# Kernel tuning notes

Measured on AMD Instinct MI355X. Metric: run time of the kernel, lower is better.

## Reference

```python
import jax, jax.numpy as jnp
import numpy as np

MARGIN = 0.2
NEG_INF = -1e9  # safe stand-in for -inf when masking the max


def setup_inputs() -> dict:
    key = jax.random.key(0)
    k1, k2, k3 = jax.random.split(key, 3)
    B, D = 8192, 256
    p = jax.random.normal(k1, (B, D), dtype=jnp.float32)
    # module docstring says projections are normalized
    projections = p / jnp.linalg.norm(p, axis=1, keepdims=True)
    affordance_ids = jax.random.randint(k2, (B,), 0, 36, dtype=jnp.int64)
    instance_ids = jax.random.randint(k3, (B,), 0, 2048, dtype=jnp.int64)
    return {
        "projections": projections,
        "affordance_ids": affordance_ids,
        "instance_ids": instance_ids,
    }


def reference(projections, affordance_ids, instance_ids):
    # (B, B) cosine similarities
    sim = jnp.matmul(projections, projections.T)

    aff_eq = affordance_ids[:, None] == affordance_ids[None, :]
    inst_eq = instance_ids[:, None] == instance_ids[None, :]
    pos_mask = aff_eq & ~inst_eq          # same affordance, different instance
    neg_mask = ~aff_eq                    # different affordance

    # per-row hard negative: max similarity over negatives
    hard_neg = jnp.max(jnp.where(neg_mask, sim, NEG_INF), axis=1)  # (B,)

    # rows contribute only if they have >=1 positive AND >=1 negative
    valid_row = pos_mask.any(axis=1) & neg_mask.any(axis=1)        # (B,)
    pair_mask = pos_mask & valid_row[:, None]                      # (B, B)

    # margin loss for every (anchor i, positive j) pair
    losses = jnp.maximum(hard_neg[:, None] - sim + MARGIN, 0.0)

    total = jnp.sum(jnp.where(pair_mask, losses, 0.0))
    num_pairs = jnp.sum(pair_mask)
    return jnp.where(num_pairs > 0, total / num_pairs, 0.0)
```

## Files before the change

### kernel.cpp

```cpp
#include <hip/hip_runtime.h>

#define NB 8192
#define ND 256
#define NCLS 64
#define LOSS_MARGIN 0.2f
#define NEG_INF_F (-1e9f)
#define LMAXT 3
#define NBLK_LOSS (NCLS * LMAXT * LMAXT)
#define NTILE_T 2080

typedef __attribute__((ext_vector_type(8))) __bf16 bf16x8;
typedef __attribute__((ext_vector_type(4))) float f32x4;

__device__ __forceinline__ unsigned short f2bf(float f) {
  unsigned u = __float_as_uint(f);
  unsigned r = (u + 0x7fffu + ((u >> 16) & 1u)) >> 16;
  return (unsigned short)r;
}

__device__ __forceinline__ void gl_lds16(const void* gsrc, void* ldst) {
  __builtin_amdgcn_global_load_lds(
      (const __attribute__((address_space(1))) void*)gsrc,
      (__attribute__((address_space(3))) void*)ldst, 16, 0, 0);
}

__global__ __launch_bounds__(1024) void build_idx_fused(const int* __restrict__ aff,
                                                        int* __restrict__ class_start,
                                                        int* __restrict__ class_idx) {
  const int c = blockIdx.x;
  const int t = threadIdx.x;
  const int lane = t & 63, wave = t >> 6;
  __shared__ int wtot[16];
  __shared__ int s_off;

  int lt = 0;
  for (int i = t; i < NB; i += 1024) lt += (aff[i] < c) ? 1 : 0;
  for (int off = 32; off; off >>= 1) lt += __shfl_down(lt, off);
  if (lane == 0) wtot[wave] = lt;
  __syncthreads();
  int base = 0;
  for (int w = 0; w < 16; ++w) base += wtot[w];
  if (t == 0) {
    class_start[c] = base;
    if (c == 0) class_start[NCLS] = NB;
  }
  __syncthreads();
  if (t == 0) s_off = 0;
  __syncthreads();

  for (int pass = 0; pass < NB / 1024; ++pass) {
    const int i = pass * 1024 + t;
    const bool m = (aff[i] == c);
    const unsigned long long mask = __ballot(m);
    if (lane == 0) wtot[wave] = __popcll(mask);
    __syncthreads();
    const int off = s_off;
    int prefix = 0;
    for (int w = 0; w < wave; ++w) prefix += wtot[w];
    if (m)
      class_idx[base + off + prefix +
                __popcll(mask & ((1ull << lane) - 1ull))] = i;
    __syncthreads();
    if (t == 0) {
      int tot = 0;
      for (int w = 0; w < 16; ++w) tot += wtot[w];
      s_off = off + tot;
    }
    __syncthreads();
  }
}

__global__ __launch_bounds__(256) void gather_convert(const float* __restrict__ P,
                                                      const int* __restrict__ aff,
                                                      const int* __restrict__ inst,
                                                      const int* __restrict__ class_idx,
                                                      unsigned short* __restrict__ Psort,
                                                      int* __restrict__ affSort,
                                                      int* __restrict__ instSort) {
  const int t = threadIdx.x;
  const int sr = blockIdx.x * 8 + (t >> 5);
  const int c = t & 31;
  const int src = class_idx[sr];
  const float4* ps = (const float4*)(P + (size_t)src * ND);
  ushort4* pd = (ushort4*)(Psort + (size_t)sr * ND);
#pragma unroll
  for (int q = 0; q < 2; ++q) {
    float4 v = ps[c + q * 32];
    ushort4 h;
    h.x = f2bf(v.x); h.y = f2bf(v.y); h.z = f2bf(v.z); h.w = f2bf(v.w);
    pd[c + q * 32] = h;
  }
  if (c == 0) {
    affSort[sr] = aff[src];
    instSort[sr] = inst[src];
  }
}

__global__ __launch_bounds__(256, 4) void simmax_mfma(const unsigned short* __restrict__ Psort,
                                                      const int* __restrict__ affSort,
                                                      float* __restrict__ part) {
  int wg = blockIdx.x;
  wg = (wg & 7) * (NTILE_T / 8) + (wg >> 3);
  int bi = (int)((129.0f - sqrtf(129.0f * 129.0f - 8.0f * (float)wg)) * 0.5f);
  while (bi * 64 - bi * (bi - 1) / 2 > wg) --bi;
  while ((bi + 1) * 64 - (bi + 1) * bi / 2 <= wg) ++bi;
  const int bj = bi + (wg - (bi * 64 - bi * (bi - 1) / 2));

  __shared__ __align__(16) unsigned short smemu[16384];
  float* rowmax_s = (float*)&smemu[0];
  float* colmax_s = (float*)&smemu[512];

  const int t = threadIdx.x;
  const int lane = t & 63;
  const int wave = t >> 6;
  const int r0 = bi * 128, c0 = bj * 128;

  const bool needMask = (affSort[c0] <= affSort[r0 + 127]);

  const int wr = (wave >> 1) * 64;
  const int wc = (wave & 1) * 64;

  f32x4 acc[4][4];
#pragma unroll
  for (int m = 0; m < 4; ++m)
#pragma unroll
    for (int n = 0; n < 4; ++n) acc[m][n] = (f32x4){0.f, 0.f, 0.f, 0.f};

  const int ci0 = t, ci1 = 256 + t;
  const int kg0 = ci0 >> 7, rw0 = ci0 & 127;
  const int kg1 = ci1 >> 7, rw1 = ci1 & 127;

#define STAGE_SIM(B, KC)                                                      \
  do {                                                                        \
    gl_lds16(Psort + (size_t)(r0 + rw0) * ND + (KC) + kg0 * 8,                \
             &smemu[(B) * 4096 + ci0 * 8]);                                   \
    gl_lds16(Psort + (size_t)(c0 + rw0) * ND + (KC) + kg0 * 8,                \
             &smemu[8192 + (B) * 4096 + ci0 * 8]);                            \
    gl_lds16(Psort + (size_t)(r0 + rw1) * ND + (KC) + kg1 * 8,                \
             &smemu[(B) * 4096 + ci1 * 8]);                                   \
    gl_lds16(Psort + (size_t)(c0 + rw1) * ND + (KC) + kg1 * 8,                \
             &smemu[8192 + (B) * 4096 + ci1 * 8]);                            \
  } while (0)

  STAGE_SIM(0, 0);
  asm volatile("s_waitcnt vmcnt(0) lgkmcnt(0)" ::: "memory");
  __builtin_amdgcn_s_barrier();
  __builtin_amdgcn_sched_barrier(0);

  int cur = 0;
#pragma unroll 1
  for (int s = 0; s < 8; ++s) {
    if (s < 7) STAGE_SIM(cur ^ 1, (s + 1) * 32);
    const int kg = lane >> 4, lr = lane & 15;
    bf16x8 a[4], b[4];
#pragma unroll
    for (int m = 0; m < 4; ++m)
      a[m] = *(const bf16x8*)&smemu[cur * 4096 + (kg * 128 + wr + m * 16 + lr) * 8];
#pragma unroll
    for (int n = 0; n < 4; ++n)
      b[n] = *(const bf16x8*)&smemu[8192 + cur * 4096 + (kg * 128 + wc + n * 16 + lr) * 8];
#pragma unroll
    for (int m = 0; m < 4; ++m)
#pragma unroll
      for (int n = 0; n < 4; ++n)
        acc[m][n] = __builtin_amdgcn_mfma_f32_16x16x32_bf16(a[m], b[n], acc[m][n], 0, 0, 0);
    __builtin_amdgcn_sched_barrier(0);
    if (s < 7) {
      asm volatile("s_waitcnt vmcnt(0)" ::: "memory");
      __builtin_amdgcn_s_barrier();
      __builtin_amdgcn_sched_barrier(0);
    }
    cur ^= 1;
  }

  if (needMask) {
#pragma unroll
    for (int m = 0; m < 4; ++m) {
#pragma unroll
      for (int r = 0; r < 4; ++r) {
        const int lrow = wr + m * 16 + (lane >> 4) * 4 + r;
        const int ai = affSort[r0 + lrow];
        float rmax = NEG_INF_F;
#pragma unroll
        for (int n = 0; n < 4; ++n) {
          const int lcol = wc + n * 16 + (lane & 15);
          if (affSort[c0 + lcol] != ai) rmax = fmaxf(rmax, acc[m][n][r]);
        }
        rmax = fmaxf(rmax, __shfl_xor(rmax, 1));
        rmax = fmaxf(rmax, __shfl_xor(rmax, 2));
        rmax = fmaxf(rmax, __shfl_xor(rmax, 4));
        rmax = fmaxf(rmax, __shfl_xor(rmax, 8));
        if ((lane & 15) == 0) rowmax_s[lrow * 2 + (wc >> 6)] = rmax;
      }
    }
    if (bi != bj) {
#pragma unroll
      for (int n = 0; n < 4; ++n) {
        const int lcol = wc + n * 16 + (lane & 15);
        const int aj = affSort[c0 + lcol];
        float cmax = NEG_INF_F;
#pragma unroll
        for (int m = 0; m < 4; ++m) {
          const int lrb = wr + m * 16 + (lane >> 4) * 4;
#pragma unroll
          for (int r = 0; r < 4; ++r)
            if (affSort[r0 + lrb + r] != aj) cmax = fmaxf(cmax, acc[m][n][r]);
        }
        cmax = fmaxf(cmax, __shfl_xor(cmax, 16));
        cmax = fmaxf(cmax, __shfl_xor(cmax, 32));
        if (lane < 16) colmax_s[lcol * 2 + (wr >> 6)] = cmax;
      }
    }
  } else {
#pragma unroll
    for (int m = 0; m < 4; ++m) {
#pragma unroll
      for (int r = 0; r < 4; ++r) {
        float rmax = fmaxf(fmaxf(acc[m][0][r], acc[m][1][r]),
                           fmaxf(acc[m][2][r], acc[m][3][r]));
        rmax = fmaxf(rmax, __shfl_xor(rmax, 1));
        rmax = fmaxf(rmax, __shfl_xor(rmax, 2));
        rmax = fmaxf(rmax, __shfl_xor(rmax, 4));
        rmax = fmaxf(rmax, __shfl_xor(rmax, 8));
        if ((lane & 15) == 0)
          rowmax_s[(wr + m * 16 + (lane >> 4) * 4 + r) * 2 + (wc >> 6)] = rmax;
      }
    }
#pragma unroll
    for (int n = 0; n < 4; ++n) {
      float cmax = NEG_INF_F;
#pragma unroll
      for (int m = 0; m < 4; ++m)
#pragma unroll
        for (int r = 0; r < 4; ++r) cmax = fmaxf(cmax, acc[m][n][r]);
      cmax = fmaxf(cmax, __shfl_xor(cmax, 16));
      cmax = fmaxf(cmax, __shfl_xor(cmax, 32));
      if (lane < 16) colmax_s[(wc + n * 16 + (lane & 15)) * 2 + (wr >> 6)] = cmax;
    }
  }
  __syncthreads();
  if (t < 128) {
    part[(size_t)bj * NB + (r0 + t)] = fmaxf(rowmax_s[t * 2], rowmax_s[t * 2 + 1]);
  } else if (bi != bj) {
    const int cc = t - 128;
    part[(size_t)bi * NB + (c0 + cc)] = fmaxf(colmax_s[cc * 2], colmax_s[cc * 2 + 1]);
  }
#undef STAGE_SIM
}

__global__ __launch_bounds__(256, 4) void loss_mfma(const unsigned short* __restrict__ Psort,
                                                    const int* __restrict__ class_start,
                                                    const int* __restrict__ instSort,
                                                    const float* __restrict__ part,
                                                    float* __restrict__ bsum,
                                                    int* __restrict__ bcnt) {
  const int c = blockIdx.z;
  const int ti = blockIdx.x, tj = blockIdx.y;
  const int bid = (c * LMAXT + ti) * LMAXT + tj;
  const int t = threadIdx.x;
  const int base = class_start[c];
  const int cnt = class_start[c + 1] - base;
  const int nt = (cnt + 127) >> 7;
  if (ti >= nt || tj >= nt || cnt >= NB) {
    if (t == 0) { bsum[bid] = 0.f; bcnt[bid] = 0; }
    return;
  }

  __shared__ __align__(16) unsigned short At[2][4096];
  __shared__ __align__(16) unsigned short Bt[2][4096];
  __shared__ int instI[128], instJ[128];
  __shared__ float hnI[128];

  const int lane = t & 63;
  const int wave = t >> 6;

  if (t < 128) {
    int ri = ti * 128 + t;
    int gi = base + (ri < cnt ? ri : 0);
    instI[t] = instSort[gi];
    float m = NEG_INF_F;
#pragma unroll 16
    for (int q = 0; q < 64; ++q) m = fmaxf(m, part[(size_t)q * NB + gi]);
    hnI[t] = m;
  } else {
    int tt = t - 128;
    int rj = tj * 128 + tt;
    int gj = base + (rj < cnt ? rj : 0);
    instJ[tt] = instSort[gj];
  }

  const int wr = (wave >> 1) * 64;
  const int wc = (wave & 1) * 64;

  f32x4 acc[4][4];
#pragma unroll
  for (int m = 0; m < 4; ++m)
#pragma unroll
    for (int n = 0; n < 4; ++n) acc[m][n] = (f32x4){0.f, 0.f, 0.f, 0.f};

  const int ci0 = t, ci1 = 256 + t;
  const int kg0 = ci0 >> 7, rw0 = ci0 & 127;
  const int kg1 = ci1 >> 7, rw1 = ci1 & 127;
  const int ra0 = base + (ti * 128 + rw0 < cnt ? ti * 128 + rw0 : 0);
  const int ra1 = base + (ti * 128 + rw1 < cnt ? ti * 128 + rw1 : 0);
  const int rb0 = base + (tj * 128 + rw0 < cnt ? tj * 128 + rw0 : 0);
  const int rb1 = base + (tj * 128 + rw1 < cnt ? tj * 128 + rw1 : 0);

#define STAGE_LOSS(B, KC)                                               \
  do {                                                                  \
    gl_lds16(Psort + (size_t)ra0 * ND + (KC) + kg0 * 8, &At[B][ci0 * 8]); \
    gl_lds16(Psort + (size_t)rb0 * ND + (KC) + kg0 * 8, &Bt[B][ci0 * 8]); \
    gl_lds16(Psort + (size_t)ra1 * ND + (KC) + kg1 * 8, &At[B][ci1 * 8]); \
    gl_lds16(Psort + (size_t)rb1 * ND + (KC) + kg1 * 8, &Bt[B][ci1 * 8]); \
  } while (0)

  STAGE_LOSS(0, 0);
  asm volatile("s_waitcnt vmcnt(0) lgkmcnt(0)" ::: "memory");
  __builtin_amdgcn_s_barrier();
  __builtin_amdgcn_sched_barrier(0);

  int cur = 0;
#pragma unroll 1
  for (int s = 0; s < 8; ++s) {
    if (s < 7) STAGE_LOSS(cur ^ 1, (s + 1) * 32);
    const int kg = lane >> 4, lr = lane & 15;
    bf16x8 a[4], b[4];
#pragma unroll
    for (int m = 0; m < 4; ++m)
      a[m] = *(const bf16x8*)&At[cur][(kg * 128 + wr + m * 16 + lr) * 8];
#pragma unroll
    for (int n = 0; n < 4; ++n)
      b[n] = *(const bf16x8*)&Bt[cur][(kg * 128 + wc + n * 16 + lr) * 8];
#pragma unroll
    for (int m = 0; m < 4; ++m)
#pragma unroll
      for (int n = 0; n < 4; ++n)
        acc[m][n] = __builtin_amdgcn_mfma_f32_16x16x32_bf16(a[m], b[n], acc[m][n], 0, 0, 0);
    __builtin_amdgcn_sched_barrier(0);
    if (s < 7) {
      asm volatile("s_waitcnt vmcnt(0)" ::: "memory");
      __builtin_amdgcn_s_barrier();
      __builtin_amdgcn_sched_barrier(0);
    }
    cur ^= 1;
  }

  float lsum = 0.f;
  int lcnt = 0;
#pragma unroll
  for (int m = 0; m < 4; ++m) {
#pragma unroll
    for (int r = 0; r < 4; ++r) {
      const int lrow = wr + m * 16 + (lane >> 4) * 4 + r;
      const int ri = ti * 128 + lrow;
      if (ri >= cnt) continue;
      const float hnv = hnI[lrow];
      const int ii = instI[lrow];
#pragma unroll
      for (int n = 0; n < 4; ++n) {
        const int lcol = wc + n * 16 + (lane & 15);
        const int rj = tj * 128 + lcol;
        if (rj < cnt && instJ[lcol] != ii) {
          lsum += fmaxf(hnv - acc[m][n][r] + LOSS_MARGIN, 0.f);
          lcnt += 1;
        }
      }
    }
  }

  for (int off = 32; off; off >>= 1) {
    lsum += __shfl_down(lsum, off);
    lcnt += __shfl_down(lcnt, off);
  }
  __shared__ float wsum[4];
  __shared__ int wcnt[4];
  if (lane == 0) { wsum[wave] = lsum; wcnt[wave] = lcnt; }
  __syncthreads();
  if (t == 0) {
    bsum[bid] = wsum[0] + wsum[1] + wsum[2] + wsum[3];
    bcnt[bid] = wcnt[0] + wcnt[1] + wcnt[2] + wcnt[3];
  }
#undef STAGE_LOSS
}

__global__ __launch_bounds__(256) void finalize_kernel(const float* __restrict__ bsum,
                                                       const int* __restrict__ bcnt,
                                                       float* __restrict__ out) {
  const int t = threadIdx.x;
  float s = 0.f;
  int n = 0;
  for (int i = t; i < NBLK_LOSS; i += 256) { s += bsum[i]; n += bcnt[i]; }
  for (int off = 32; off; off >>= 1) {
    s += __shfl_down(s, off);
    n += __shfl_down(n, off);
  }
  __shared__ float wsum[4];
  __shared__ int wcnt[4];
  if ((t & 63) == 0) { wsum[t >> 6] = s; wcnt[t >> 6] = n; }
  __syncthreads();
  if (t == 0) {
    const float S = wsum[0] + wsum[1] + wsum[2] + wsum[3];
    const int N = wcnt[0] + wcnt[1] + wcnt[2] + wcnt[3];
    out[0] = (N > 0) ? (S / (float)N) : 0.0f;
  }
}

extern "C" void kernel_launch(void* const* d_in, const int* in_sizes, int n_in,
                              void* d_out, int out_size, void* d_ws, size_t ws_size,
                              hipStream_t stream) {
  const float* P = (const float*)d_in[0];
  const int* aff = (const int*)d_in[1];
  const int* inst = (const int*)d_in[2];
  float* out = (float*)d_out;

  unsigned short* Psort = (unsigned short*)d_ws;
  float* part = (float*)((char*)d_ws + (size_t)NB * ND * 2);
  int* ibase = (int*)((char*)part + (size_t)64 * NB * 4);
  int* class_start = ibase;
  int* class_idx   = ibase + NCLS + 1;
  int* affSort     = ibase + NCLS + 1 + NB;
  int* instSort    = ibase + NCLS + 1 + 2 * NB;
  float* bsum = (float*)(ibase + NCLS + 1 + 3 * NB);
  int* bcnt   = ibase + NCLS + 1 + 3 * NB + NBLK_LOSS;

  build_idx_fused<<<NCLS, 1024, 0, stream>>>(aff, class_start, class_idx);
  gather_convert<<<NB / 8, 256, 0, stream>>>(P, aff, inst, class_idx, Psort,
                                             affSort, instSort);
  simmax_mfma<<<NTILE_T, 256, 0, stream>>>(Psort, affSort, part);
  loss_mfma<<<dim3(LMAXT, LMAXT, NCLS), 256, 0, stream>>>(Psort, class_start, instSort,
                                                          part, bsum, bcnt);
  finalize_kernel<<<1, 256, 0, stream>>>(bsum, bcnt, out);
}
```

Baseline: 93.04 us.

## Enlarge simmax tiles to 256x256 with 512-thread workgroups

Doubles the symmetric similarity tile from 128 to 256 rows/cols, using 8 waves each computing a 128x64 sub-tile, which halves the number of upper-triangular tiles and the per-row partial-max array (32 instead of 64 slices). This raises operand reuse per LDS load and reduces global traffic for partials and the loss kernel's reduction over them. In exchange it uses twice the LDS and more accumulator registers per thread, and launches far fewer workgroups (528), which may underfill the GPU and lower occupancy.

```diff
diff --git a/kernel.cpp b/kernel.cpp
--- a/kernel.cpp
+++ b/kernel.cpp
@@ -7,7 +7,8 @@
 #define NEG_INF_F (-1e9f)
 #define LMAXT 3
 #define NBLK_LOSS (NCLS * LMAXT * LMAXT)
-#define NTILE_T 2080
+#define NT 32
+#define NTILE_T 528
 
 typedef __attribute__((ext_vector_type(8))) __bf16 bf16x8;
 typedef __attribute__((ext_vector_type(4))) float f32x4;
@@ -96,50 +97,49 @@
   }
 }
 
-__global__ __launch_bounds__(256, 4) void simmax_mfma(const unsigned short* __restrict__ Psort,
-                                                      const int* __restrict__ affSort,
-                                                      float* __restrict__ part) {
+__global__ __launch_bounds__(512) void simmax_mfma(const unsigned short* __restrict__ Psort,
+                                                   const int* __restrict__ affSort,
+                                                   float* __restrict__ part) {
   int wg = blockIdx.x;
   wg = (wg & 7) * (NTILE_T / 8) + (wg >> 3);
-  int bi = (int)((129.0f - sqrtf(129.0f * 129.0f - 8.0f * (float)wg)) * 0.5f);
-  while (bi * 64 - bi * (bi - 1) / 2 > wg) --bi;
-  while ((bi + 1) * 64 - (bi + 1) * bi / 2 <= wg) ++bi;
-  const int bj = bi + (wg - (bi * 64 - bi * (bi - 1) / 2));
-
-  __shared__ __align__(16) unsigned short smemu[16384];
+  int bi = (int)((65.0f - sqrtf(65.0f * 65.0f - 8.0f * (float)wg)) * 0.5f);
+  while (bi * (65 - bi) / 2 > wg) --bi;
+  while ((bi + 1) * (64 - bi) / 2 <= wg) ++bi;
+  const int bj = bi + (wg - bi * (65 - bi) / 2);
+
+  __shared__ __align__(16) unsigned short smemu[32768];
   float* rowmax_s = (float*)&smemu[0];
-  float* colmax_s = (float*)&smemu[512];
+  float* colmax_s = (float*)&smemu[2048];
 
   const int t = threadIdx.x;
   const int lane = t & 63;
   const int wave = t >> 6;
-  const int r0 = bi * 128, c0 = bj * 128;
-
-  const bool needMask = (affSort[c0] <= affSort[r0 + 127]);
-
-  const int wr = (wave >> 1) * 64;
-  const int wc = (wave & 1) * 64;
-
-  f32x4 acc[4][4];
-#pragma unroll
-  for (int m = 0; m < 4; ++m)
+  const int r0 = bi * 256, c0 = bj * 256;
+
+  const bool needMask = (affSort[c0] <= affSort[r0 + 255]);
+
+  const int wr = (wave >> 2) * 128;
+  const int wc = (wave & 3) * 64;
+
+  f32x4 acc[8][4];
+#pragma unroll
+  for (int m = 0; m < 8; ++m)
 #pragma unroll
     for (int n = 0; n < 4; ++n) acc[m][n] = (f32x4){0.f, 0.f, 0.f, 0.f};
 
-  const int ci0 = t, ci1 = 256 + t;
-  const int kg0 = ci0 >> 7, rw0 = ci0 & 127;
-  const int kg1 = ci1 >> 7, rw1 = ci1 & 127;
-
-#define STAGE_SIM(B, KC)                                                      \
-  do {                                                                        \
-    gl_lds16(Psort + (size_t)(r0 + rw0) * ND + (KC) + kg0 * 8,                \
-             &smemu[(B) * 4096 + ci0 * 8]);                                   \
-    gl_lds16(Psort + (size_t)(c0 + rw0) * ND + (KC) + kg0 * 8,                \
-             &smemu[8192 + (B) * 4096 + ci0 * 8]);                            \
-    gl_lds16(Psort + (size_t)(r0 + rw1) * ND + (KC) + kg1 * 8,                \
-             &smemu[(B) * 4096 + ci1 * 8]);                                   \
-    gl_lds16(Psort + (size_t)(c0 + rw1) * ND + (KC) + kg1 * 8,                \
-             &smemu[8192 + (B) * 4096 + ci1 * 8]);                            \
+  const int kg0 = t >> 8, rw0 = t & 255;
+  const int kg1 = 2 + (t >> 8), rw1 = t & 255;
+
+#define STAGE_SIM(B, KC)                                                       \
+  do {                                                                         \
+    gl_lds16(Psort + (size_t)(r0 + rw0) * ND + (KC) + kg0 * 8,                 \
+             &smemu[(B) * 8192 + t * 8]);                                      \
+    gl_lds16(Psort + (size_t)(r0 + rw1) * ND + (KC) + kg1 * 8,                 \
+             &smemu[(B) * 8192 + (512 + t) * 8]);                              \
+    gl_lds16(Psort + (size_t)(c0 + rw0) * ND + (KC) + kg0 * 8,                 \
+             &smemu[16384 + (B) * 8192 + t * 8]);                              \
+    gl_lds16(Psort + (size_t)(c0 + rw1) * ND + (KC) + kg1 * 8,                 \
+             &smemu[16384 + (B) * 8192 + (512 + t) * 8]);                      \
   } while (0)
 
   STAGE_SIM(0, 0);
@@ -152,15 +152,15 @@
   for (int s = 0; s < 8; ++s) {
     if (s < 7) STAGE_SIM(cur ^ 1, (s + 1) * 32);
     const int kg = lane >> 4, lr = lane & 15;
-    bf16x8 a[4], b[4];
-#pragma unroll
-    for (int m = 0; m < 4; ++m)
-      a[m] = *(const bf16x8*)&smemu[cur * 4096 + (kg * 128 + wr + m * 16 + lr) * 8];
+    bf16x8 a[8], b[4];
+#pragma unroll
+    for (int m = 0; m < 8; ++m)
+      a[m] = *(const bf16x8*)&smemu[cur * 8192 + (kg * 256 + wr + m * 16 + lr) * 8];
 #pragma unroll
     for (int n = 0; n < 4; ++n)
-      b[n] = *(const bf16x8*)&smemu[8192 + cur * 4096 + (kg * 128 + wc + n * 16 + lr) * 8];
-#pragma unroll
-    for (int m = 0; m < 4; ++m)
+      b[n] = *(const bf16x8*)&smemu[16384 + cur * 8192 + (kg * 256 + wc + n * 16 + lr) * 8];
+#pragma unroll
+    for (int m = 0; m < 8; ++m)
 #pragma unroll
       for (int n = 0; n < 4; ++n)
         acc[m][n] = __builtin_amdgcn_mfma_f32_16x16x32_bf16(a[m], b[n], acc[m][n], 0, 0, 0);
@@ -174,46 +174,46 @@
   }
 
   if (needMask) {
-#pragma unroll
-    for (int m = 0; m < 4; ++m) {
+    int aj[4];
+#pragma unroll
+    for (int n = 0; n < 4; ++n) aj[n] = affSort[c0 + wc + n * 16 + (lane & 15)];
+#pragma unroll
+    for (int m = 0; m < 8; ++m) {
 #pragma unroll
       for (int r = 0; r < 4; ++r) {
         const int lrow = wr + m * 16 + (lane >> 4) * 4 + r;
         const int ai = affSort[r0 + lrow];
         float rmax = NEG_INF_F;
 #pragma unroll
-        for (int n = 0; n < 4; ++n) {
-          const int lcol = wc + n * 16 + (lane & 15);
-          if (affSort[c0 + lcol] != ai) rmax = fmaxf(rmax, acc[m][n][r]);
-        }
+        for (int n = 0; n < 4; ++n)
+          if (aj[n] != ai) rmax = fmaxf(rmax, acc[m][n][r]);
         rmax = fmaxf(rmax, __shfl_xor(rmax, 1));
         rmax = fmaxf(rmax, __shfl_xor(rmax, 2));
         rmax = fmaxf(rmax, __shfl_xor(rmax, 4));
         rmax = fmaxf(rmax, __shfl_xor(rmax, 8));
-        if ((lane & 15) == 0) rowmax_s[lrow * 2 + (wc >> 6)] = rmax;
+        if ((lane & 15) == 0) rowmax_s[lrow * 4 + (wave & 3)] = rmax;
       }
     }
     if (bi != bj) {
 #pragma unroll
       for (int n = 0; n < 4; ++n) {
         const int lcol = wc + n * 16 + (lane & 15);
-        const int aj = affSort[c0 + lcol];
         float cmax = NEG_INF_F;
 #pragma unroll
-        for (int m = 0; m < 4; ++m) {
+        for (int m = 0; m < 8; ++m) {
           const int lrb = wr + m * 16 + (lane >> 4) * 4;
 #pragma unroll
           for (int r = 0; r < 4; ++r)
-            if (affSort[r0 + lrb + r] != aj) cmax = fmaxf(cmax, acc[m][n][r]);
+            if (affSort[r0 + lrb + r] != aj[n]) cmax = fmaxf(cmax, acc[m][n][r]);
         }
         cmax = fmaxf(cmax, __shfl_xor(cmax, 16));
         cmax = fmaxf(cmax, __shfl_xor(cmax, 32));
-        if (lane < 16) colmax_s[lcol * 2 + (wr >> 6)] = cmax;
+        if (lane < 16) colmax_s[lcol * 2 + (wave >> 2)] = cmax;
       }
     }
   } else {
 #pragma unroll
-    for (int m = 0; m < 4; ++m) {
+    for (int m = 0; m < 8; ++m) {
 #pragma unroll
       for (int r = 0; r < 4; ++r) {
         float rmax = fmaxf(fmaxf(acc[m][0][r], acc[m][1][r]),
@@ -223,26 +223,28 @@
         rmax = fmaxf(rmax, __shfl_xor(rmax, 4));
         rmax = fmaxf(rmax, __shfl_xor(rmax, 8));
         if ((lane & 15) == 0)
-          rowmax_s[(wr + m * 16 + (lane >> 4) * 4 + r) * 2 + (wc >> 6)] = rmax;
+          rowmax_s[(wr + m * 16 + (lane >> 4) * 4 + r) * 4 + (wave & 3)] = rmax;
       }
     }
 #pragma unroll
     for (int n = 0; n < 4; ++n) {
       float cmax = NEG_INF_F;
 #pragma unroll
-      for (int m = 0; m < 4; ++m)
+      for (int m = 0; m < 8; ++m)
 #pragma unroll
         for (int r = 0; r < 4; ++r) cmax = fmaxf(cmax, acc[m][n][r]);
       cmax = fmaxf(cmax, __shfl_xor(cmax, 16));
       cmax = fmaxf(cmax, __shfl_xor(cmax, 32));
-      if (lane < 16) colmax_s[(wc + n * 16 + (lane & 15)) * 2 + (wr >> 6)] = cmax;
-    }
-  }
-  __syncthreads();
-  if (t < 128) {
-    part[(size_t)bj * NB + (r0 + t)] = fmaxf(rowmax_s[t * 2], rowmax_s[t * 2 + 1]);
+      if (lane < 16) colmax_s[(wc + n * 16 + (lane & 15)) * 2 + (wave >> 2)] = cmax;
+    }
+  }
+  __syncthreads();
+  if (t < 256) {
+    const float* r = &rowmax_s[t * 4];
+    part[(size_t)bj * NB + (r0 + t)] =
+        fmaxf(fmaxf(r[0], r[1]), fmaxf(r[2], r[3]));
   } else if (bi != bj) {
-    const int cc = t - 128;
+    const int cc = t - 256;
     part[(size_t)bi * NB + (c0 + cc)] = fmaxf(colmax_s[cc * 2], colmax_s[cc * 2 + 1]);
   }
 #undef STAGE_SIM
@@ -279,8 +281,8 @@
     int gi = base + (ri < cnt ? ri : 0);
     instI[t] = instSort[gi];
     float m = NEG_INF_F;
-#pragma unroll 16
-    for (int q = 0; q < 64; ++q) m = fmaxf(m, part[(size_t)q * NB + gi]);
+#pragma unroll 8
+    for (int q = 0; q < NT; ++q) m = fmaxf(m, part[(size_t)q * NB + gi]);
     hnI[t] = m;
   } else {
     int tt = t - 128;
@@ -415,7 +417,7 @@
 
   unsigned short* Psort = (unsigned short*)d_ws;
   float* part = (float*)((char*)d_ws + (size_t)NB * ND * 2);
-  int* ibase = (int*)((char*)part + (size_t)64 * NB * 4);
+  int* ibase = (int*)((char*)part + (size_t)NT * NB * 4);
   int* class_start = ibase;
   int* class_idx   = ibase + NCLS + 1;
   int* affSort     = ibase + NCLS + 1 + NB;
@@ -426,7 +428,7 @@
   build_idx_fused<<<NCLS, 1024, 0, stream>>>(aff, class_start, class_idx);
   gather_convert<<<NB / 8, 256, 0, stream>>>(P, aff, inst, class_idx, Psort,
                                              affSort, instSort);
-  simmax_mfma<<<NTILE_T, 256, 0, stream>>>(Psort, affSort, part);
+  simmax_mfma<<<NTILE_T, 512, 0, stream>>>(Psort, affSort, part);
   loss_mfma<<<dim3(LMAXT, LMAXT, NCLS), 256, 0, stream>>>(Psort, class_start, instSort,
                                                           part, bsum, bcnt);
   finalize_kernel<<<1, 256, 0, stream>>>(bsum, bcnt, out);
```

After: 101.5 us. 9.0% more time.

## Load MFMA operands directly from global memory instead of LDS double-buffering

Applied to the files above, without the earlier changes.

Both GEMM-style kernels drop the global_load_lds double-buffered shared-memory staging and barrier pipeline. Each wave now reads its bf16x8 A/B fragments straight from global memory into registers, relying on L1/L2 caches. This removes LDS usage and per-stage barriers, and frees the compiler to schedule loads freely. The cost is duplicated global traffic across waves, since fragments are no longer shared through LDS, and less coalesced row-strided 16-byte loads. The occupancy hint is also dropped, and an explicit __syncthreads is added in the loss kernel to replace the barrier that staging used to provide.

```diff
diff --git a/kernel.cpp b/kernel.cpp
--- a/kernel.cpp
+++ b/kernel.cpp
@@ -7,6 +7,7 @@
 #define NEG_INF_F (-1e9f)
 #define LMAXT 3
 #define NBLK_LOSS (NCLS * LMAXT * LMAXT)
+#define NT 64
 #define NTILE_T 2080
 
 typedef __attribute__((ext_vector_type(8))) __bf16 bf16x8;
@@ -16,12 +17,6 @@
   unsigned u = __float_as_uint(f);
   unsigned r = (u + 0x7fffu + ((u >> 16) & 1u)) >> 16;
   return (unsigned short)r;
-}
-
-__device__ __forceinline__ void gl_lds16(const void* gsrc, void* ldst) {
-  __builtin_amdgcn_global_load_lds(
-      (const __attribute__((address_space(1))) void*)gsrc,
-      (__attribute__((address_space(3))) void*)ldst, 16, 0, 0);
 }
 
 __global__ __launch_bounds__(1024) void build_idx_fused(const int* __restrict__ aff,
@@ -96,9 +91,9 @@
   }
 }
 
-__global__ __launch_bounds__(256, 4) void simmax_mfma(const unsigned short* __restrict__ Psort,
-                                                      const int* __restrict__ affSort,
-                                                      float* __restrict__ part) {
+__global__ __launch_bounds__(256) void simmax_mfma(const unsigned short* __restrict__ Psort,
+                                                   const int* __restrict__ affSort,
+                                                   float* __restrict__ part) {
   int wg = blockIdx.x;
   wg = (wg & 7) * (NTILE_T / 8) + (wg >> 3);
   int bi = (int)((129.0f - sqrtf(129.0f * 129.0f - 8.0f * (float)wg)) * 0.5f);
@@ -106,9 +101,8 @@
   while ((bi + 1) * 64 - (bi + 1) * bi / 2 <= wg) ++bi;
   const int bj = bi + (wg - (bi * 64 - bi * (bi - 1) / 2));
 
-  __shared__ __align__(16) unsigned short smemu[16384];
-  float* rowmax_s = (float*)&smemu[0];
-  float* colmax_s = (float*)&smemu[512];
+  __shared__ float rowmax_s[128][2];
+  __shared__ float colmax_s[128][2];
 
   const int t = threadIdx.x;
   const int lane = t & 63;
@@ -119,6 +113,16 @@
 
   const int wr = (wave >> 1) * 64;
   const int wc = (wave & 1) * 64;
+  const int lr = lane & 15, kg = lane >> 4;
+
+  const unsigned short* pa[4];
+  const unsigned short* pb[4];
+#pragma unroll
+  for (int m = 0; m < 4; ++m)
+    pa[m] = Psort + (size_t)(r0 + wr + m * 16 + lr) * ND + kg * 8;
+#pragma unroll
+  for (int n = 0; n < 4; ++n)
+    pb[n] = Psort + (size_t)(c0 + wc + n * 16 + lr) * ND + kg * 8;
 
   f32x4 acc[4][4];
 #pragma unroll
@@ -126,54 +130,24 @@
 #pragma unroll
     for (int n = 0; n < 4; ++n) acc[m][n] = (f32x4){0.f, 0.f, 0.f, 0.f};
 
-  const int ci0 = t, ci1 = 256 + t;
-  const int kg0 = ci0 >> 7, rw0 = ci0 & 127;
-  const int kg1 = ci1 >> 7, rw1 = ci1 & 127;
-
-#define STAGE_SIM(B, KC)                                                      \
-  do {                                                                        \
-    gl_lds16(Psort + (size_t)(r0 + rw0) * ND + (KC) + kg0 * 8,                \
-             &smemu[(B) * 4096 + ci0 * 8]);                                   \
-    gl_lds16(Psort + (size_t)(c0 + rw0) * ND + (KC) + kg0 * 8,                \
-             &smemu[8192 + (B) * 4096 + ci0 * 8]);                            \
-    gl_lds16(Psort + (size_t)(r0 + rw1) * ND + (KC) + kg1 * 8,                \
-             &smemu[(B) * 4096 + ci1 * 8]);                                   \
-    gl_lds16(Psort + (size_t)(c0 + rw1) * ND + (KC) + kg1 * 8,                \
-             &smemu[8192 + (B) * 4096 + ci1 * 8]);                            \
-  } while (0)
-
-  STAGE_SIM(0, 0);
-  asm volatile("s_waitcnt vmcnt(0) lgkmcnt(0)" ::: "memory");
-  __builtin_amdgcn_s_barrier();
-  __builtin_amdgcn_sched_barrier(0);
-
-  int cur = 0;
-#pragma unroll 1
-  for (int s = 0; s < 8; ++s) {
-    if (s < 7) STAGE_SIM(cur ^ 1, (s + 1) * 32);
-    const int kg = lane >> 4, lr = lane & 15;
+#pragma unroll
+  for (int kc = 0; kc < ND; kc += 32) {
     bf16x8 a[4], b[4];
 #pragma unroll
-    for (int m = 0; m < 4; ++m)
-      a[m] = *(const bf16x8*)&smemu[cur * 4096 + (kg * 128 + wr + m * 16 + lr) * 8];
-#pragma unroll
-    for (int n = 0; n < 4; ++n)
-      b[n] = *(const bf16x8*)&smemu[8192 + cur * 4096 + (kg * 128 + wc + n * 16 + lr) * 8];
+    for (int m = 0; m < 4; ++m) a[m] = *(const bf16x8*)(pa[m] + kc);
+#pragma unroll
+    for (int n = 0; n < 4; ++n) b[n] = *(const bf16x8*)(pb[n] + kc);
 #pragma unroll
     for (int m = 0; m < 4; ++m)
 #pragma unroll
       for (int n = 0; n < 4; ++n)
         acc[m][n] = __builtin_amdgcn_mfma_f32_16x16x32_bf16(a[m], b[n], acc[m][n], 0, 0, 0);
-    __builtin_amdgcn_sched_barrier(0);
-    if (s < 7) {
-      asm volatile("s_waitcnt vmcnt(0)" ::: "memory");
-      __builtin_amdgcn_s_barrier();
-      __builtin_amdgcn_sched_barrier(0);
-    }
-    cur ^= 1;
   }
 
   if (needMask) {
+    int aj[4];
+#pragma unroll
+    for (int n = 0; n < 4; ++n) aj[n] = affSort[c0 + wc + n * 16 + (lane & 15)];
 #pragma unroll
     for (int m = 0; m < 4; ++m) {
 #pragma unroll
@@ -182,33 +156,30 @@
         const int ai = affSort[r0 + lrow];
         float rmax = NEG_INF_F;
 #pragma unroll
-        for (int n = 0; n < 4; ++n) {
-          const int lcol = wc + n * 16 + (lane & 15);
-          if (affSort[c0 + lcol] != ai) rmax = fmaxf(rmax, acc[m][n][r]);
-        }
+        for (int n = 0; n < 4; ++n)
+          if (aj[n] != ai) rmax = fmaxf(rmax, acc[m][n][r]);
         rmax = fmaxf(rmax, __shfl_xor(rmax, 1));
         rmax = fmaxf(rmax, __shfl_xor(rmax, 2));
         rmax = fmaxf(rmax, __shfl_xor(rmax, 4));
         rmax = fmaxf(rmax, __shfl_xor(rmax, 8));
-        if ((lane & 15) == 0) rowmax_s[lrow * 2 + (wc >> 6)] = rmax;
+        if ((lane & 15) == 0) rowmax_s[lrow][wc >> 6] = rmax;
       }
     }
     if (bi != bj) {
 #pragma unroll
       for (int n = 0; n < 4; ++n) {
         const int lcol = wc + n * 16 + (lane & 15);
-        const int aj = affSort[c0 + lcol];
         float cmax = NEG_INF_F;
 #pragma unroll
         for (int m = 0; m < 4; ++m) {
           const int lrb = wr + m * 16 + (lane >> 4) * 4;
 #pragma unroll
           for (int r = 0; r < 4; ++r)
-            if (affSort[r0 + lrb + r] != aj) cmax = fmaxf(cmax, acc[m][n][r]);
+            if (affSort[r0 + lrb + r] != aj[n]) cmax = fmaxf(cmax, acc[m][n][r]);
         }
         cmax = fmaxf(cmax, __shfl_xor(cmax, 16));
         cmax = fmaxf(cmax, __shfl_xor(cmax, 32));
-        if (lane < 16) colmax_s[lcol * 2 + (wr >> 6)] = cmax;
+        if (lane < 16) colmax_s[lcol][wr >> 6] = cmax;
       }
     }
   } else {
@@ -223,7 +194,7 @@
         rmax = fmaxf(rmax, __shfl_xor(rmax, 4));
         rmax = fmaxf(rmax, __shfl_xor(rmax, 8));
         if ((lane & 15) == 0)
-          rowmax_s[(wr + m * 16 + (lane >> 4) * 4 + r) * 2 + (wc >> 6)] = rmax;
+          rowmax_s[wr + m * 16 + (lane >> 4) * 4 + r][wc >> 6] = rmax;
       }
     }
 #pragma unroll
@@ -235,25 +206,24 @@
         for (int r = 0; r < 4; ++r) cmax = fmaxf(cmax, acc[m][n][r]);
       cmax = fmaxf(cmax, __shfl_xor(cmax, 16));
       cmax = fmaxf(cmax, __shfl_xor(cmax, 32));
-      if (lane < 16) colmax_s[(wc + n * 16 + (lane & 15)) * 2 + (wr >> 6)] = cmax;
+      if (lane < 16) colmax_s[wc + n * 16 + (lane & 15)][wr >> 6] = cmax;
     }
   }
   __syncthreads();
   if (t < 128) {
-    part[(size_t)bj * NB + (r0 + t)] = fmaxf(rowmax_s[t * 2], rowmax_s[t * 2 + 1]);
+    part[(size_t)bj * NB + (r0 + t)] = fmaxf(rowmax_s[t][0], rowmax_s[t][1]);
   } else if (bi != bj) {
     const int cc = t - 128;
-    part[(size_t)bi * NB + (c0 + cc)] = fmaxf(colmax_s[cc * 2], colmax_s[cc * 2 + 1]);
-  }
-#undef STAGE_SIM
-}
-
-__global__ __launch_bounds__(256, 4) void loss_mfma(const unsigned short* __restrict__ Psort,
-                                                    const int* __restrict__ class_start,
-                                                    const int* __restrict__ instSort,
-                                                    const float* __restrict__ part,
-                                                    float* __restrict__ bsum,
-                                                    int* __restrict__ bcnt) {
+    part[(size_t)bi * NB + (c0 + cc)] = fmaxf(colmax_s[cc][0], colmax_s[cc][1]);
+  }
+}
+
+__global__ __launch_bounds__(256) void loss_mfma(const unsigned short* __restrict__ Psort,
+                                                 const int* __restrict__ class_start,
+                                                 const int* __restrict__ instSort,
+                                                 const float* __restrict__ part,
+                                                 float* __restrict__ bsum,
+                                                 int* __restrict__ bcnt) {
   const int c = blockIdx.z;
   const int ti = blockIdx.x, tj = blockIdx.y;
   const int bid = (c * LMAXT + ti) * LMAXT + tj;
@@ -266,8 +236,6 @@
     return;
   }
 
-  __shared__ __align__(16) unsigned short At[2][4096];
-  __shared__ __align__(16) unsigned short Bt[2][4096];
   __shared__ int instI[128], instJ[128];
   __shared__ float hnI[128];
 
@@ -280,7 +248,7 @@
     instI[t] = instSort[gi];
     float m = NEG_INF_F;
 #pragma unroll 16
-    for (int q = 0; q < 64; ++q) m = fmaxf(m, part[(size_t)q * NB + gi]);
+    for (int q = 0; q < NT; ++q) m = fmaxf(m, part[(size_t)q * NB + gi]);
     hnI[t] = m;
   } else {
     int tt = t - 128;
@@ -288,9 +256,24 @@
     int gj = base + (rj < cnt ? rj : 0);
     instJ[tt] = instSort[gj];
   }
+  __syncthreads();
 
   const int wr = (wave >> 1) * 64;
   const int wc = (wave & 1) * 64;
+  const int lr = lane & 15, kg = lane >> 4;
+
+  const unsigned short* pa[4];
+  const unsigned short* pb[4];
+#pragma unroll
+  for (int m = 0; m < 4; ++m) {
+    int rr = ti * 128 + wr + m * 16 + lr;
+    pa[m] = Psort + (size_t)(base + (rr < cnt ? rr : 0)) * ND + kg * 8;
+  }
+#pragma unroll
+  for (int n = 0; n < 4; ++n) {
+    int rc = tj * 128 + wc + n * 16 + lr;
+    pb[n] = Psort + (size_t)(base + (rc < cnt ? rc : 0)) * ND + kg * 8;
+  }
 
   f32x4 acc[4][4];
 #pragma unroll
@@ -298,51 +281,18 @@
 #pragma unroll
     for (int n = 0; n < 4; ++n) acc[m][n] = (f32x4){0.f, 0.f, 0.f, 0.f};
 
-  const int ci0 = t, ci1 = 256 + t;
-  const int kg0 = ci0 >> 7, rw0 = ci0 & 127;
-  const int kg1 = ci1 >> 7, rw1 = ci1 & 127;
-  const int ra0 = base + (ti * 128 + rw0 < cnt ? ti * 128 + rw0 : 0);
-  const int ra1 = base + (ti * 128 + rw1 < cnt ? ti * 128 + rw1 : 0);
-  const int rb0 = base + (tj * 128 + rw0 < cnt ? tj * 128 + rw0 : 0);
-  const int rb1 = base + (tj * 128 + rw1 < cnt ? tj * 128 + rw1 : 0);
-
-#define STAGE_LOSS(B, KC)                                               \
-  do {                                                                  \
-    gl_lds16(Psort + (size_t)ra0 * ND + (KC) + kg0 * 8, &At[B][ci0 * 8]); \
-    gl_lds16(Psort + (size_t)rb0 * ND + (KC) + kg0 * 8, &Bt[B][ci0 * 8]); \
-    gl_lds16(Psort + (size_t)ra1 * ND + (KC) + kg1 * 8, &At[B][ci1 * 8]); \
-    gl_lds16(Psort + (size_t)rb1 * ND + (KC) + kg1 * 8, &Bt[B][ci1 * 8]); \
-  } while (0)
-
-  STAGE_LOSS(0, 0);
-  asm volatile("s_waitcnt vmcnt(0) lgkmcnt(0)" ::: "memory");
-  __builtin_amdgcn_s_barrier();
-  __builtin_amdgcn_sched_barrier(0);
-
-  int cur = 0;
-#pragma unroll 1
-  for (int s = 0; s < 8; ++s) {
-    if (s < 7) STAGE_LOSS(cur ^ 1, (s + 1) * 32);
-    const int kg = lane >> 4, lr = lane & 15;
+#pragma unroll
+  for (int kc = 0; kc < ND; kc += 32) {
     bf16x8 a[4], b[4];
 #pragma unroll
-    for (int m = 0; m < 4; ++m)
-      a[m] = *(const bf16x8*)&At[cur][(kg * 128 + wr + m * 16 + lr) * 8];
-#pragma unroll
-    for (int n = 0; n < 4; ++n)
-      b[n] = *(const bf16x8*)&Bt[cur][(kg * 128 + wc + n * 16 + lr) * 8];
+    for (int m = 0; m < 4; ++m) a[m] = *(const bf16x8*)(pa[m] + kc);
+#pragma unroll
+    for (int n = 0; n < 4; ++n) b[n] = *(const bf16x8*)(pb[n] + kc);
 #pragma unroll
     for (int m = 0; m < 4; ++m)
 #pragma unroll
       for (int n = 0; n < 4; ++n)
         acc[m][n] = __builtin_amdgcn_mfma_f32_16x16x32_bf16(a[m], b[n], acc[m][n], 0, 0, 0);
-    __builtin_amdgcn_sched_barrier(0);
-    if (s < 7) {
-      asm volatile("s_waitcnt vmcnt(0)" ::: "memory");
-      __builtin_amdgcn_s_barrier();
-      __builtin_amdgcn_sched_barrier(0);
-    }
-    cur ^= 1;
   }
 
   float lsum = 0.f;
@@ -380,7 +330,6 @@
     bsum[bid] = wsum[0] + wsum[1] + wsum[2] + wsum[3];
     bcnt[bid] = wcnt[0] + wcnt[1] + wcnt[2] + wcnt[3];
   }
-#undef STAGE_LOSS
 }
 
 __global__ __launch_bounds__(256) void finalize_kernel(const float* __restrict__ bsum,
@@ -415,7 +364,7 @@
 
   unsigned short* Psort = (unsigned short*)d_ws;
   float* part = (float*)((char*)d_ws + (size_t)NB * ND * 2);
-  int* ibase = (int*)((char*)part + (size_t)64 * NB * 4);
+  int* ibase = (int*)((char*)part + (size_t)NT * NB * 4);
   int* class_start = ibase;
   int* class_idx   = ibase + NCLS + 1;
   int* affSort     = ibase + NCLS + 1 + NB;
```

New measurement: 134.1 us. 44.2% more time.

## Triple-buffer simmax K-loop and split hard-negative reduction into separate kernel

Applied to the files above, without the earlier changes.

Replaces the double-buffered LDS pipeline in simmax_mfma with a triple-buffered, fully unrolled K loop that keeps two stages in flight. This lets global-to-LDS loads overlap more with MFMA work and removes one barrier per step. The launch_bounds occupancy hint is dropped and LDS use grows to 48KB, which may lower occupancy. The per-row max over 64 partial columns moves out of loss_mfma into a small hn_reduce kernel, so it is computed once per row rather than redundantly in each loss tile. Affinity column values are also hoisted into registers in the mask epilogue.

```diff
diff --git a/kernel.cpp b/kernel.cpp
--- a/kernel.cpp
+++ b/kernel.cpp
@@ -7,6 +7,7 @@
 #define NEG_INF_F (-1e9f)
 #define LMAXT 3
 #define NBLK_LOSS (NCLS * LMAXT * LMAXT)
+#define NT 64
 #define NTILE_T 2080
 
 typedef __attribute__((ext_vector_type(8))) __bf16 bf16x8;
@@ -96,9 +97,9 @@
   }
 }
 
-__global__ __launch_bounds__(256, 4) void simmax_mfma(const unsigned short* __restrict__ Psort,
-                                                      const int* __restrict__ affSort,
-                                                      float* __restrict__ part) {
+__global__ __launch_bounds__(256) void simmax_mfma(const unsigned short* __restrict__ Psort,
+                                                   const int* __restrict__ affSort,
+                                                   float* __restrict__ part) {
   int wg = blockIdx.x;
   wg = (wg & 7) * (NTILE_T / 8) + (wg >> 3);
   int bi = (int)((129.0f - sqrtf(129.0f * 129.0f - 8.0f * (float)wg)) * 0.5f);
@@ -106,7 +107,7 @@
   while ((bi + 1) * 64 - (bi + 1) * bi / 2 <= wg) ++bi;
   const int bj = bi + (wg - (bi * 64 - bi * (bi - 1) / 2));
 
-  __shared__ __align__(16) unsigned short smemu[16384];
+  __shared__ __align__(16) unsigned short smemu[24576];
   float* rowmax_s = (float*)&smemu[0];
   float* colmax_s = (float*)&smemu[512];
 
@@ -135,45 +136,54 @@
     gl_lds16(Psort + (size_t)(r0 + rw0) * ND + (KC) + kg0 * 8,                \
              &smemu[(B) * 4096 + ci0 * 8]);                                   \
     gl_lds16(Psort + (size_t)(c0 + rw0) * ND + (KC) + kg0 * 8,                \
-             &smemu[8192 + (B) * 4096 + ci0 * 8]);                            \
+             &smemu[12288 + (B) * 4096 + ci0 * 8]);                           \
     gl_lds16(Psort + (size_t)(r0 + rw1) * ND + (KC) + kg1 * 8,                \
              &smemu[(B) * 4096 + ci1 * 8]);                                   \
     gl_lds16(Psort + (size_t)(c0 + rw1) * ND + (KC) + kg1 * 8,                \
-             &smemu[8192 + (B) * 4096 + ci1 * 8]);                            \
+             &smemu[12288 + (B) * 4096 + ci1 * 8]);                           \
   } while (0)
 
+#define KSTEP_SIM(S, VM)                                                      \
+  do {                                                                        \
+    asm volatile("s_waitcnt vmcnt(" #VM ")" ::: "memory");                    \
+    __builtin_amdgcn_s_barrier();                                             \
+    __builtin_amdgcn_sched_barrier(0);                                        \
+    if ((S) + 2 < 8) STAGE_SIM(((S) + 2) % 3, ((S) + 2) * 32);                \
+    const int kg = lane >> 4, lr = lane & 15;                                 \
+    bf16x8 a[4], b[4];                                                        \
+    _Pragma("unroll")                                                         \
+    for (int m = 0; m < 4; ++m)                                               \
+      a[m] = *(const bf16x8*)&smemu[((S) % 3) * 4096 +                        \
+                                    (kg * 128 + wr + m * 16 + lr) * 8];       \
+    _Pragma("unroll")                                                         \
+    for (int n = 0; n < 4; ++n)                                               \
+      b[n] = *(const bf16x8*)&smemu[12288 + ((S) % 3) * 4096 +                \
+                                    (kg * 128 + wc + n * 16 + lr) * 8];       \
+    _Pragma("unroll")                                                         \
+    for (int m = 0; m < 4; ++m)                                               \
+      _Pragma("unroll")                                                       \
+      for (int n = 0; n < 4; ++n)                                             \
+        acc[m][n] = __builtin_amdgcn_mfma_f32_16x16x32_bf16(a[m], b[n],       \
+                                                            acc[m][n], 0, 0, 0); \
+    __builtin_amdgcn_sched_barrier(0);                                        \
+  } while (0)
+
   STAGE_SIM(0, 0);
-  asm volatile("s_waitcnt vmcnt(0) lgkmcnt(0)" ::: "memory");
-  __builtin_amdgcn_s_barrier();
-  __builtin_amdgcn_sched_barrier(0);
-
-  int cur = 0;
-#pragma unroll 1
-  for (int s = 0; s < 8; ++s) {
-    if (s < 7) STAGE_SIM(cur ^ 1, (s + 1) * 32);
-    const int kg = lane >> 4, lr = lane & 15;
-    bf16x8 a[4], b[4];
-#pragma unroll
-    for (int m = 0; m < 4; ++m)
-      a[m] = *(const bf16x8*)&smemu[cur * 4096 + (kg * 128 + wr + m * 16 + lr) * 8];
-#pragma unroll
-    for (int n = 0; n < 4; ++n)
-      b[n] = *(const bf16x8*)&smemu[8192 + cur * 4096 + (kg * 128 + wc + n * 16 + lr) * 8];
-#pragma unroll
-    for (int m = 0; m < 4; ++m)
-#pragma unroll
-      for (int n = 0; n < 4; ++n)
-        acc[m][n] = __builtin_amdgcn_mfma_f32_16x16x32_bf16(a[m], b[n], acc[m][n], 0, 0, 0);
-    __builtin_amdgcn_sched_barrier(0);
-    if (s < 7) {
-      asm volatile("s_waitcnt vmcnt(0)" ::: "memory");
-      __builtin_amdgcn_s_barrier();
-      __builtin_amdgcn_sched_barrier(0);
-    }
-    cur ^= 1;
-  }
+  STAGE_SIM(1, 32);
+
+  KSTEP_SIM(0, 4);
+  KSTEP_SIM(1, 4);
+  KSTEP_SIM(2, 4);
+  KSTEP_SIM(3, 4);
+  KSTEP_SIM(4, 4);
+  KSTEP_SIM(5, 4);
+  KSTEP_SIM(6, 4);
+  KSTEP_SIM(7, 0);
 
   if (needMask) {
+    int aj[4];
+#pragma unroll
+    for (int n = 0; n < 4; ++n) aj[n] = affSort[c0 + wc + n * 16 + (lane & 15)];
 #pragma unroll
     for (int m = 0; m < 4; ++m) {
 #pragma unroll
@@ -182,10 +192,8 @@
         const int ai = affSort[r0 + lrow];
         float rmax = NEG_INF_F;
 #pragma unroll
-        for (int n = 0; n < 4; ++n) {
-          const int lcol = wc + n * 16 + (lane & 15);
-          if (affSort[c0 + lcol] != ai) rmax = fmaxf(rmax, acc[m][n][r]);
-        }
+        for (int n = 0; n < 4; ++n)
+          if (aj[n] != ai) rmax = fmaxf(rmax, acc[m][n][r]);
         rmax = fmaxf(rmax, __shfl_xor(rmax, 1));
         rmax = fmaxf(rmax, __shfl_xor(rmax, 2));
         rmax = fmaxf(rmax, __shfl_xor(rmax, 4));
@@ -197,14 +205,13 @@
 #pragma unroll
       for (int n = 0; n < 4; ++n) {
         const int lcol = wc + n * 16 + (lane & 15);
-        const int aj = affSort[c0 + lcol];
         float cmax = NEG_INF_F;
 #pragma unroll
         for (int m = 0; m < 4; ++m) {
           const int lrb = wr + m * 16 + (lane >> 4) * 4;
 #pragma unroll
           for (int r = 0; r < 4; ++r)
-            if (affSort[r0 + lrb + r] != aj) cmax = fmaxf(cmax, acc[m][n][r]);
+            if (affSort[r0 + lrb + r] != aj[n]) cmax = fmaxf(cmax, acc[m][n][r]);
         }
         cmax = fmaxf(cmax, __shfl_xor(cmax, 16));
         cmax = fmaxf(cmax, __shfl_xor(cmax, 32));
@@ -245,13 +252,23 @@
     const int cc = t - 128;
     part[(size_t)bi * NB + (c0 + cc)] = fmaxf(colmax_s[cc * 2], colmax_s[cc * 2 + 1]);
   }
+#undef KSTEP_SIM
 #undef STAGE_SIM
+}
+
+__global__ __launch_bounds__(256) void hn_reduce(const float* __restrict__ part,
+                                                 float* __restrict__ hn) {
+  const int i = blockIdx.x * 256 + threadIdx.x;
+  float m = NEG_INF_F;
+#pragma unroll 16
+  for (int q = 0; q < NT; ++q) m = fmaxf(m, part[(size_t)q * NB + i]);
+  hn[i] = m;
 }
 
 __global__ __launch_bounds__(256, 4) void loss_mfma(const unsigned short* __restrict__ Psort,
                                                     const int* __restrict__ class_start,
                                                     const int* __restrict__ instSort,
-                                                    const float* __restrict__ part,
+                                                    const float* __restrict__ hn,
                                                     float* __restrict__ bsum,
                                                     int* __restrict__ bcnt) {
   const int c = blockIdx.z;
@@ -278,10 +295,7 @@
     int ri = ti * 128 + t;
     int gi = base + (ri < cnt ? ri : 0);
     instI[t] = instSort[gi];
-    float m = NEG_INF_F;
-#pragma unroll 16
-    for (int q = 0; q < 64; ++q) m = fmaxf(m, part[(size_t)q * NB + gi]);
-    hnI[t] = m;
+    hnI[t] = hn[gi];
   } else {
     int tt = t - 128;
     int rj = tj * 128 + tt;
@@ -415,19 +429,21 @@
 
   unsigned short* Psort = (unsigned short*)d_ws;
   float* part = (float*)((char*)d_ws + (size_t)NB * ND * 2);
-  int* ibase = (int*)((char*)part + (size_t)64 * NB * 4);
-  int* class_start = ibase;
-  int* class_idx   = ibase + NCLS + 1;
-  int* affSort     = ibase + NCLS + 1 + NB;
-  int* instSort    = ibase + NCLS + 1 + 2 * NB;
-  float* bsum = (float*)(ibase + NCLS + 1 + 3 * NB);
-  int* bcnt   = ibase + NCLS + 1 + 3 * NB + NBLK_LOSS;
+  int* ibase = (int*)((char*)part + (size_t)NT * NB * 4);
+  float* hn        = (float*)ibase;
+  int* class_start = ibase + NB;
+  int* class_idx   = ibase + NB + NCLS + 1;
+  int* affSort     = ibase + 2 * NB + NCLS + 1;
+  int* instSort    = ibase + 3 * NB + NCLS + 1;
+  float* bsum = (float*)(ibase + 4 * NB + NCLS + 1);
+  int* bcnt   = ibase + 4 * NB + NCLS + 1 + NBLK_LOSS;
 
   build_idx_fused<<<NCLS, 1024, 0, stream>>>(aff, class_start, class_idx);
   gather_convert<<<NB / 8, 256, 0, stream>>>(P, aff, inst, class_idx, Psort,
                                              affSort, instSort);
   simmax_mfma<<<NTILE_T, 256, 0, stream>>>(Psort, affSort, part);
+  hn_reduce<<<NB / 256, 256, 0, stream>>>(part, hn);
   loss_mfma<<<dim3(LMAXT, LMAXT, NCLS), 256, 0, stream>>>(Psort, class_start, instSort,
-                                                          part, bsum, bcnt);
+                                                          hn, bsum, bcnt);
   finalize_kernel<<<1, 256, 0, stream>>>(bsum, bcnt, out);
 }
```

After: 98.97 us. 1.06x slower.
